# Kernel tuning notes

Measured on AMD Instinct MI355X. Metric: run time of the kernel, lower is better.

## Reference

```python
import jax, jax.numpy as jnp
import numpy as np

N_SAMPLES = 131072
N_EVENTS = 128
N_ATOMS = 32
ATOM_SIZE = 512
LATENT_DIM = 16
TOTAL_LAYERS = 7  # log2(n_events)


def setup_inputs() -> dict:
    key = jax.random.key(0)
    ks = jax.random.split(key, 9)
    r = lambda k, s: jax.random.normal(k, s, dtype=jnp.float32) * 0.1
    return {
        "base_latent": r(ks[0], (1, LATENT_DIM)),
        "to_off_w": r(ks[1], (TOTAL_LAYERS, 2, LATENT_DIM)),
        "split_w": r(ks[2], (TOTAL_LAYERS, 2 * LATENT_DIM, LATENT_DIM)),
        "split_b": r(ks[3], (TOTAL_LAYERS, 2 * LATENT_DIM)),
        "atoms": r(ks[4], (N_ATOMS, ATOM_SIZE)),
        "to_atoms_w": r(ks[5], (N_ATOMS, LATENT_DIM)),
        "to_atoms_b": r(ks[6], (N_ATOMS,)),
        "to_amp_w": r(ks[7], (1, LATENT_DIM)),
        "to_amp_b": r(ks[8], (1,)),
    }


def fft_shift(a, shift):
    # FFT-based fractional delay: pad to 3*n, phase-rotate spectrum, crop.
    n = a.shape[-1]
    shift_samples = shift * n * 0.5  # shift: (B, E, 1)
    a = jnp.pad(a, [(0, 0)] * (a.ndim - 1) + [(0, n * 2)])
    spec = jnp.fft.rfft(a, axis=-1, norm="ortho")
    n_coeffs = spec.shape[-1]
    coeffs = (jnp.arange(n_coeffs) * 2j * jnp.pi) / n_coeffs  # (n_coeffs,)
    spec = spec * jnp.exp(coeffs * shift_samples)  # broadcast (B,E,n_coeffs)
    samples = jnp.fft.irfft(spec, axis=-1, norm="ortho")
    return samples[..., :n]


def _forward(base_latent, to_off_w, split_w, split_b, atoms,
             to_atoms_w, to_atoms_b, to_amp_w, to_amp_b):
    x = base_latent[:, None, :]                     # (1, 1, L)
    base_times = jnp.zeros((1, 1, 1), dtype=x.dtype)
    for i in range(TOTAL_LAYERS):
        scale = 1.0 / (2 ** i)
        b, e, _ = x.shape
        to = jax.nn.sigmoid(jnp.einsum("bel,ol->beo", x, to_off_w[i]))  # (b,e,2)
        base_times = (base_times + to * scale).reshape(b, e * 2, 1)
        split = jnp.einsum("bel,ol->beo", x, split_w[i]) + split_b[i]   # (b,e,2L)
        x = split.reshape(b, e * 2, LATENT_DIM)
    # x: (1, 128, L), base_times: (1, 128, 1)
    mix = jnp.einsum("bel,al->bea", x, to_atoms_w) + to_atoms_b          # (1,E,A)
    ev = jnp.einsum("bea,at->bet", mix, atoms)                           # (1,E,512)
    n_arr = jnp.arange(ATOM_SIZE, dtype=ev.dtype)
    window = 0.54 - 0.46 * jnp.cos(2.0 * jnp.pi * n_arr / ATOM_SIZE)     # periodic hamming
    ev = ev * window
    ev = jnp.pad(ev, ((0, 0), (0, 0), (0, N_SAMPLES - ATOM_SIZE)))       # (1,E,n_samples)
    ev = ev / (jnp.linalg.norm(ev, axis=-1, keepdims=True) + 1e-8)       # unit_norm
    amps = jnp.einsum("bel,ol->beo", x, to_amp_w) + to_amp_b             # (1,E,1)
    ev = ev * amps
    scheduled = fft_shift(ev, base_times)                                # (1,E,n_samples)
    return jnp.sum(scheduled, axis=1, keepdims=True)                     # (1,1,n_samples)


def reference(base_latent, to_off_w, split_w, split_b, atoms,
              to_atoms_w, to_atoms_b, to_amp_w, to_amp_b):
    return _forward(base_latent, to_off_w, split_w, split_b, atoms,
                    to_atoms_w, to_atoms_b, to_amp_w, to_amp_b)
```

## Files before the change

### kernel.cpp

```cpp
#include <hip/hip_runtime.h>
#include <hip/hip_bf16.h>
#include <math.h>

constexpr int NSAMP  = 131072;
constexpr int NEV    = 128;
constexpr int ASIZE  = 512;
constexpr int LDIM   = 16;
constexpr int NLAYER = 7;
constexpr int NFFT   = 393216;
constexpr int MHALF  = 196608;
constexpr double TWO_PI = 6.283185307179586;


__device__ __forceinline__ float2 cmulf(float2 a, float2 b) {
    return make_float2(a.x*b.x - a.y*b.y, a.x*b.y + a.y*b.x);
}
__device__ __forceinline__ float2 CADD(float2 a, float2 b){ return make_float2(a.x+b.x, a.y+b.y); }
__device__ __forceinline__ float2 CSUB(float2 a, float2 b){ return make_float2(a.x-b.x, a.y-b.y); }

__device__ __forceinline__ void phase_sc(float th32, float* ps, float* pc) {
    const double th = (double)th32;
    const double n  = rint(th * 0.15915494309189535);
    double r = fma(-n, 6.283185307179586, th);
    r = fma(-n, 2.4492935982947064e-16, r);
    __sincosf((float)r, ps, pc);
}

#define RT2 0.70710678118654752f
#define DFT8F(A0,A1,A2,A3,A4,A5,A6,A7, X0,X1,X2,X3,X4,X5,X6,X7) { \
  float2 b0=CADD(A0,A4), b1=CADD(A1,A5), b2=CADD(A2,A6), b3=CADD(A3,A7); \
  float2 c0=CSUB(A0,A4); \
  float2 d1=CSUB(A1,A5), d2=CSUB(A2,A6), d3=CSUB(A3,A7); \
  float2 c1=make_float2((d1.x+d1.y)*RT2, (d1.y-d1.x)*RT2); \
  float2 c2=make_float2(d2.y, -d2.x); \
  float2 c3=make_float2((d3.y-d3.x)*RT2, -(d3.x+d3.y)*RT2); \
  float2 t0=CADD(b0,b2), t1=CSUB(b0,b2), t2=CADD(b1,b3), t3=CSUB(b1,b3); \
  X0=CADD(t0,t2); X4=CSUB(t0,t2); \
  X2=make_float2(t1.x+t3.y, t1.y-t3.x); X6=make_float2(t1.x-t3.y, t1.y+t3.x); \
  t0=CADD(c0,c2); t1=CSUB(c0,c2); t2=CADD(c1,c3); t3=CSUB(c1,c3); \
  X1=CADD(t0,t2); X5=CSUB(t0,t2); \
  X3=make_float2(t1.x+t3.y, t1.y-t3.x); X7=make_float2(t1.x-t3.y, t1.y+t3.x); \
}

__global__ __launch_bounds__(256) void init_all(
    const float* __restrict__ base, const float* __restrict__ to_off_w,
    const float* __restrict__ split_w, const float* __restrict__ split_b,
    float* __restrict__ xF, float* __restrict__ sF,
    float2* __restrict__ Twf, float2* __restrict__ Ttab)
{
    const int blk = blockIdx.x;
    const int tid = threadIdx.x;
    if (blk == 0) {
        __shared__ float xA[NEV*LDIM], xB[NEV*LDIM], bA[NEV], bB[NEV];
        if (tid < LDIM) xA[tid] = base[tid];
        if (tid == 0) bA[0] = 0.0f;
        __syncthreads();
        float* xi = xA; float* xo = xB; float* bi = bA; float* bo = bB;
        for (int i = 0; i < NLAYER; ++i) {
            const int ein = 1 << i;
            const float scale = 1.0f / (float)(1 << i);
            for (int idx = tid; idx < ein*32; idx += 256) {
                const int ep = idx >> 5, o2 = idx & 31;
                const float* wr = split_w + (i*32 + o2)*LDIM;
                const float* xr = xi + ep*LDIM;
                float s = __fmul_rn(xr[0], wr[0]);
                for (int l = 1; l < LDIM; ++l)
                    s = __fadd_rn(s, __fmul_rn(xr[l], wr[l]));
                s = __fadd_rn(s, split_b[i*32 + o2]);
                xo[(ep*2 + (o2>>4))*LDIM + (o2&15)] = s;
            }
            for (int idx = tid; idx < ein*2; idx += 256) {
                const int ep = idx >> 1, o = idx & 1;
                const float* wr = to_off_w + (i*2 + o)*LDIM;
                const float* xr = xi + ep*LDIM;
                float v = __fmul_rn(xr[0], wr[0]);
                for (int l = 1; l < LDIM; ++l)
                    v = __fadd_rn(v, __fmul_rn(xr[l], wr[l]));
                const float ef = (float)exp(-(double)v);
                const float sg = __fdiv_rn(1.0f, __fadd_rn(1.0f, ef));
                bo[ep*2 + o] = __fadd_rn(bi[ep], __fmul_rn(sg, scale));
            }
            __syncthreads();
            float* t;
            t = xi; xi = xo; xo = t;
            t = bi; bi = bo; bo = t;
        }
        for (int idx = tid; idx < NEV*LDIM; idx += 256) xF[idx] = xi[idx];
        for (int e = tid; e < NEV; e += 256)
            sF[e] = __fmul_rn(__fmul_rn(bi[e], 131072.0f), 0.5f);
        return;
    }
    if (blk == 1) {
        double s, c;
        sincos(TWO_PI*(double)tid/256.0,   &s, &c); Twf[tid]       = make_float2((float)c,(float)s);
        sincos(TWO_PI*(double)tid/512.0,   &s, &c); Twf[256 + tid] = make_float2((float)c,(float)s);
        sincos(TWO_PI*(double)tid/768.0,   &s, &c); Twf[512 + tid] = make_float2((float)c,(float)s);
        sincos(TWO_PI*(double)tid/65536.0, &s, &c); Twf[768 + tid] = make_float2((float)c,(float)s);
        return;
    }
    const int b = blk - 2;
    for (int j = tid; j < 512; j += 256) {
        double s, c;
        sincos(-TWO_PI*(double)(b*j)/(double)NFFT, &s, &c);
        Ttab[b*512 + j] = make_float2((float)c, (float)s);
    }
}

__global__ __launch_bounds__(256) void events_f32(
    const float* __restrict__ atoms, const float* __restrict__ to_atoms_w,
    const float* __restrict__ to_atoms_b, const float* __restrict__ to_amp_w,
    const float* __restrict__ to_amp_b, const float* __restrict__ xF,
    float* __restrict__ zf)
{
    const int e = blockIdx.x;
    const int tid = threadIdx.x;
    __shared__ float mixS[32];
    __shared__ float evS[ASIZE];
    __shared__ double red[256];
    __shared__ float scl[2];
    const float* x = xF + e*LDIM;
    if (tid < 32) {
        const float* wr = to_atoms_w + tid*LDIM;
        float m = __fmul_rn(x[0], wr[0]);
        for (int l = 1; l < LDIM; ++l) m = __fadd_rn(m, __fmul_rn(x[l], wr[l]));
        mixS[tid] = __fadd_rn(m, to_atoms_b[tid]);
    }
    __syncthreads();
    double ss = 0.0;
    for (int u = tid; u < ASIZE; u += 256) {
        float v = __fmul_rn(mixS[0], atoms[u]);
        for (int a = 1; a < 32; ++a)
            v = __fadd_rn(v, __fmul_rn(mixS[a], atoms[a*ASIZE + u]));
        const float ang = __fdiv_rn(__fmul_rn(6.283185307179586f, (float)u), 512.0f);
        const float cw = (float)cos((double)ang);
        const float w  = __fsub_rn(0.54f, __fmul_rn(0.46f, cw));
        v = __fmul_rn(v, w);
        evS[u] = v;
        ss += (double)v * (double)v;
    }
    red[tid] = ss; __syncthreads();
    for (int s = 128; s > 0; s >>= 1) { if (tid < s) red[tid] += red[tid+s]; __syncthreads(); }
    if (tid == 0) {
        const float nf = (float)sqrt(red[0]);
        scl[0] = __fadd_rn(nf, 1e-8f);
        float a = __fmul_rn(x[0], to_amp_w[0]);
        for (int l = 1; l < LDIM; ++l) a = __fadd_rn(a, __fmul_rn(x[l], to_amp_w[l]));
        scl[1] = __fadd_rn(a, to_amp_b[0]);
    }
    __syncthreads();
    const float den = scl[0], amp = scl[1];
    for (int u = tid; u < ASIZE; u += 256)
        zf[e*ASIZE + u] = __fmul_rn(__fdiv_rn(evS[u], den), amp);
}

__global__ __launch_bounds__(256, 3) void forward_v2(
    const float* __restrict__ zf, const float* __restrict__ sF,
    const float2* __restrict__ Ttab, float* __restrict__ Hqf)
{
    __shared__ float2 FB[4*576];
    __shared__ float  sSh[32];
    const int b       = blockIdx.x >> 2;
    const int quarter = blockIdx.x & 3;
    const int tid  = threadIdx.x;
    const int wave = tid >> 6, lane = tid & 63;
    float2* F = FB + wave*576;
    const int e0 = quarter*32;
    const float2* Tg = Ttab + b*512;

    if (tid < 32) sSh[tid] = sF[e0 + tid];
    __syncthreads();

    float2 w0b, w1b;
    __sincosf(-6.283185307179586f/512.0f * (float)lane,        &w0b.y, &w0b.x);
    __sincosf(-6.283185307179586f/64.0f  * (float)(lane >> 3), &w1b.y, &w1b.x);

    float c2a[4], c2b[4];
    #pragma unroll
    for (int j = 0; j < 4; ++j) {
        const int a  = lane + 64*j;
        const int k1 = b + 768*a;
        const int k2 = (768 - b) + 768*(255 - a);
        c2a[j] = __fdiv_rn(__fmul_rn((float)(2*k1), 3.14159274101257324f), 196609.0f);
        c2b[j] = __fdiv_rn(__fmul_rn((float)(2*k2), 3.14159274101257324f), 196609.0f);
    }

    float a1R[4]={0,0,0,0}, a1I[4]={0,0,0,0};
    float a2R[4]={0,0,0,0}, a2I[4]={0,0,0,0};
    const int ph = lane + (lane >> 3);

    for (int it = 0; it < 8; ++it) {
        const int e = e0 + wave*8 + it;
        const float* zp = zf + e*ASIZE;
        {
            float2 i0,i1,i2,i3,i4,i5,i6,i7;
            {
                float z; float2 tt;
                z = zp[lane      ]; tt = Tg[lane      ]; i0 = make_float2(z*tt.x, z*tt.y);
                z = zp[lane +  64]; tt = Tg[lane +  64]; i1 = make_float2(z*tt.x, z*tt.y);
                z = zp[lane + 128]; tt = Tg[lane + 128]; i2 = make_float2(z*tt.x, z*tt.y);
                z = zp[lane + 192]; tt = Tg[lane + 192]; i3 = make_float2(z*tt.x, z*tt.y);
                z = zp[lane + 256]; tt = Tg[lane + 256]; i4 = make_float2(z*tt.x, z*tt.y);
                z = zp[lane + 320]; tt = Tg[lane + 320]; i5 = make_float2(z*tt.x, z*tt.y);
                z = zp[lane + 384]; tt = Tg[lane + 384]; i6 = make_float2(z*tt.x, z*tt.y);
                z = zp[lane + 448]; tt = Tg[lane + 448]; i7 = make_float2(z*tt.x, z*tt.y);
            }
            float2 x0,x1,x2,x3,x4,x5,x6,x7;
            DFT8F(i0,i1,i2,i3,i4,i5,i6,i7, x0,x1,x2,x3,x4,x5,x6,x7);
            const int ob = 9*lane;
            float2 wm = w0b;
            F[ob]   = x0;
            F[ob+1] = cmulf(x1, wm); wm = cmulf(wm, w0b);
            F[ob+2] = cmulf(x2, wm); wm = cmulf(wm, w0b);
            F[ob+3] = cmulf(x3, wm); wm = cmulf(wm, w0b);
            F[ob+4] = cmulf(x4, wm); wm = cmulf(wm, w0b);
            F[ob+5] = cmulf(x5, wm); wm = cmulf(wm, w0b);
            F[ob+6] = cmulf(x6, wm); wm = cmulf(wm, w0b);
            F[ob+7] = cmulf(x7, wm);
        }
        {
            const float2 i0 = F[ph      ], i1 = F[ph +  72], i2 = F[ph + 144],
                         i3 = F[ph + 216], i4 = F[ph + 288], i5 = F[ph + 360],
                         i6 = F[ph + 432], i7 = F[ph + 504];
            float2 x0,x1,x2,x3,x4,x5,x6,x7;
            DFT8F(i0,i1,i2,i3,i4,i5,i6,i7, x0,x1,x2,x3,x4,x5,x6,x7);
            const int q = lane & 7, p = lane >> 3;
            const int ob = q + 72*p;
            float2 wm = w1b;
            F[ob]    = x0;
            F[ob+ 9] = cmulf(x1, wm); wm = cmulf(wm, w1b);
            F[ob+18] = cmulf(x2, wm); wm = cmulf(wm, w1b);
            F[ob+27] = cmulf(x3, wm); wm = cmulf(wm, w1b);
            F[ob+36] = cmulf(x4, wm); wm = cmulf(wm, w1b);
            F[ob+45] = cmulf(x5, wm); wm = cmulf(wm, w1b);
            F[ob+54] = cmulf(x6, wm); wm = cmulf(wm, w1b);
            F[ob+63] = cmulf(x7, wm);
        }
        float2 Y[8];
        {
            const float2 i0 = F[ph      ], i1 = F[ph +  72], i2 = F[ph + 144],
                         i3 = F[ph + 216], i4 = F[ph + 288], i5 = F[ph + 360],
                         i6 = F[ph + 432], i7 = F[ph + 504];
            DFT8F(i0,i1,i2,i3,i4,i5,i6,i7, Y[0],Y[1],Y[2],Y[3],Y[4],Y[5],Y[6],Y[7]);
        }
        const float se = sSh[wave*8 + it];
        #pragma unroll
        for (int j = 0; j < 4; ++j) {
            float ps, pc;
            const float2 S0 = Y[j];
            phase_sc(__fmul_rn(c2a[j], se), &ps, &pc);
            a1R[j] = fmaf(S0.x, pc, fmaf(-S0.y, ps, a1R[j]));
            a1I[j] = fmaf(S0.x, ps, fmaf( S0.y, pc, a1I[j]));
            const float2 S1 = Y[j+4];
            phase_sc(__fmul_rn(c2b[j], se), &ps, &pc);
            a2R[j] = fmaf(S1.x, pc, fmaf( S1.y, ps, a2R[j]));
            a2I[j] = fmaf(S1.x, ps, fmaf(-S1.y, pc, a2I[j]));
        }
    }

    float* redF = (float*)FB;
    #pragma unroll
    for (int round = 0; round < 2; ++round) {
        __syncthreads();
        const int j0 = 2*round;
        float* my = redF + (wave*64 + lane)*8;
        my[0]=a1R[j0];   my[1]=a1I[j0];   my[2]=a2R[j0];   my[3]=a2I[j0];
        my[4]=a1R[j0+1]; my[5]=a1I[j0+1]; my[6]=a2R[j0+1]; my[7]=a2I[j0+1];
        __syncthreads();
        const int s = tid >> 2, c = tid & 3;
        #pragma unroll
        for (int jr = 0; jr < 2; ++jr) {
            float v = 0.f;
            #pragma unroll
            for (int w = 0; w < 4; ++w) v += redF[(w*64 + s)*8 + jr*4 + c];
            const int as = s + 64*(j0 + jr);
            if (c < 2) {
                Hqf[2*(quarter*196609 + b*256 + as) + c] = v;
            } else if (b != 384) {
                if (b != 0)
                    Hqf[2*(quarter*196609 + (768-b)*256 + (255-as)) + (c-2)] = v;
                else if (as == 0)
                    Hqf[2*(quarter*196609 + 196608) + (c-2)] = v;
            }
        }
    }
}

__device__ __forceinline__ void ifft256f_stage(
    const float2* __restrict__ src, float2* __restrict__ dst, int t, int s4,
    const float2* __restrict__ Tw256f)
{
    const int lg = 2*s4, st = 1 << lg;
    const int q = t & (st-1), p = t >> lg;
    const float2 A0 = src[t], A1 = src[t+64], A2 = src[t+128], A3 = src[t+192];
    const float Pr = A0.x + A2.x, Pi_ = A0.y + A2.y;
    const float Qr = A0.x - A2.x, Qi  = A0.y - A2.y;
    const float Rr = A1.x + A3.x, Ri  = A1.y + A3.y;
    const float Sr = A1.x - A3.x, Si  = A1.y - A3.y;
    const int tw = p*st;
    const float2 w1 = Tw256f[tw];
    const float2 w2 = Tw256f[(2*tw) & 255];
    const float2 w3 = Tw256f[(3*tw) & 255];
    const int o = q + 4*st*p;
    dst[o] = make_float2(Pr + Rr, Pi_ + Ri);
    const float u1r = Qr - Si, u1i = Qi + Sr;
    dst[o + st]   = make_float2(u1r*w1.x - u1i*w1.y, u1r*w1.y + u1i*w1.x);
    const float u2r = Pr - Rr, u2i = Pi_ - Ri;
    dst[o + 2*st] = make_float2(u2r*w2.x - u2i*w2.y, u2r*w2.y + u2i*w2.x);
    const float u3r = Qr + Si, u3i = Qi - Sr;
    dst[o + 3*st] = make_float2(u3r*w3.x - u3i*w3.y, u3r*w3.y + u3i*w3.x);
}

__global__ __launch_bounds__(64) void inv_a(
    const float* __restrict__ Hqf, const float2* __restrict__ Twf,
    float2* __restrict__ Yg)
{
    __shared__ float2 buf[512];
    const int t = threadIdx.x;
    const int job = blockIdx.x;
    const int l = job >> 8, j1 = job & 255;
    const int k0 = 3*j1 + l;
    float2* A = buf; float2* B = buf + 256;
    const float2* Hq2 = (const float2*)Hqf;
    const float2* Tw256f = Twf;
    const float2* Tw512f = Twf + 256;
    const float2* Tw64kf = Twf + 768;

    double Ss, Sc; sincos(TWO_PI*(double)k0/(double)NFFT, &Ss, &Sc);
    const float Scf = (float)Sc, Ssf = (float)Ss;

    #pragma unroll
    for (int r = 0; r < 4; ++r) {
        const int j2 = t + 64*r;
        const int idxK = k0*256 + j2;
        int idxM;
        if (k0 > 0) idxM = (768 - k0)*256 + (255 - j2);
        else        idxM = (j2 == 0) ? 196608 : (256 - j2);
        float hkR=0.f, hkI=0.f, hmR=0.f, hmI=0.f;
        #pragma unroll
        for (int q = 0; q < 4; ++q) {
            const float2 vk = Hq2[q*196609 + idxK];
            const float2 vm = Hq2[q*196609 + idxM];
            hkR += vk.x; hkI += vk.y;
            hmR += vm.x; hmI += vm.y;
        }
        if (k0 == 0 && j2 == 0) { hkI = 0.f; hmI = 0.f; }
        const float Pr = hkR + hmR, Pi_ = hkI - hmI;
        const float Qr = hkR - hmR, Qi = hkI + hmI;
        const float2 t5 = Tw512f[j2];
        const float Wc = Scf*t5.x - Ssf*t5.y;
        const float Wsn = Scf*t5.y + Ssf*t5.x;
        const float WQr = Wc*Qr - Wsn*Qi;
        const float WQi = Wc*Qi + Wsn*Qr;
        A[j2] = make_float2(0.5f*(Pr - WQi), 0.5f*(Pi_ + WQr));
    }

    ifft256f_stage(A, B, t, 0, Tw256f);
    ifft256f_stage(B, A, t, 1, Tw256f);
    ifft256f_stage(A, B, t, 2, Tw256f);
    ifft256f_stage(B, A, t, 3, Tw256f);

    #pragma unroll
    for (int r = 0; r < 4; ++r) {
        const int m1 = t + 64*r;
        const float2 v = A[m1];
        const int vv = j1*m1;
        const float2 wa = Tw256f[vv >> 8];
        const float2 wb = Tw64kf[vv & 255];
        const float twc = wa.x*wb.x - wa.y*wb.y;
        const float tws = wa.x*wb.y + wa.y*wb.x;
        Yg[m1*768 + job] = make_float2(v.x*twc - v.y*tws, v.x*tws + v.y*twc);
    }
}

__global__ __launch_bounds__(192) void inv_b(
    const float2* __restrict__ Yg, const float2* __restrict__ Twf,
    float* __restrict__ out)
{
    __shared__ float2 buf[3*512];
    const int m1 = blockIdx.x;
    const int tid = threadIdx.x;
    const int l = tid >> 6, t = tid & 63;
    const float2* Tw256f = Twf;
    const float2* Tw768f = Twf + 512;
    {
        float2* A = buf + l*512;
        float2* B = A + 256;
        #pragma unroll
        for (int r = 0; r < 4; ++r) {
            const int j1 = t + 64*r;
            A[j1] = Yg[m1*768 + l*256 + j1];
        }
        ifft256f_stage(A, B, t, 0, Tw256f);
        ifft256f_stage(B, A, t, 1, Tw256f);
        ifft256f_stage(A, B, t, 2, Tw256f);
        ifft256f_stage(B, A, t, 3, Tw256f);
    }
    __syncthreads();

    double smd, cmd; sincos(TWO_PI*(double)m1/(double)MHALF, &smd, &cmd);
    const float cm = (float)cmd, sm = (float)smd;
    const float inv = 1.0f/(float)MHALF;
    for (int m2 = tid; m2 < 256; m2 += 192) {
        const float2 F0 = buf[m2];
        const float2 F1 = buf[512 + m2];
        const float2 F2 = buf[1024 + m2];
        const float2 t7 = Tw768f[m2];
        const float w1c = cm*t7.x - sm*t7.y, w1s = cm*t7.y + sm*t7.x;
        const float w2c = w1c*w1c - w1s*w1s, w2s = 2.0f*w1c*w1s;
        const float gr = F0.x + (w1c*F1.x - w1s*F1.y) + (w2c*F2.x - w2s*F2.y);
        const float gi = F0.y + (w1c*F1.y + w1s*F1.x) + (w2c*F2.y + w2s*F2.x);
        const int m = m1 + 256*m2;
        out[2*m]     = gr*inv;
        out[2*m + 1] = gi*inv;
    }
}

extern "C" void kernel_launch(void* const* d_in, const int* in_sizes, int n_in,
                              void* d_out, int out_size, void* d_ws, size_t ws_size,
                              hipStream_t stream) {
    const float* base       = (const float*)d_in[0];
    const float* to_off_w   = (const float*)d_in[1];
    const float* split_w    = (const float*)d_in[2];
    const float* split_b    = (const float*)d_in[3];
    const float* atoms      = (const float*)d_in[4];
    const float* to_atoms_w = (const float*)d_in[5];
    const float* to_atoms_b = (const float*)d_in[6];
    const float* to_amp_w   = (const float*)d_in[7];
    const float* to_amp_b   = (const float*)d_in[8];
    float* out = (float*)d_out;

    char* ws = (char*)d_ws;
    float2* Twf  = (float2*)(ws + 0);
    float*  sF   = (float*)(ws + 8192);
    float*  xF   = (float*)(ws + 8704);
    float*  zf   = (float*)(ws + 16896);
    float2* Ttab = (float2*)(ws + 279040);
    float2* Yg   = (float2*)(ws + 279040);
    float*  Hqf  = (float*)(ws + 1856000);

    init_all<<<387, 256, 0, stream>>>(base, to_off_w, split_w, split_b,
                                      xF, sF, Twf, Ttab);
    events_f32<<<NEV, 256, 0, stream>>>(atoms, to_atoms_w, to_atoms_b,
                                        to_amp_w, to_amp_b, xF, zf);
    forward_v2<<<385*4, 256, 0, stream>>>(zf, sF, Ttab, Hqf);
    inv_a<<<768, 64, 0, stream>>>(Hqf, Twf, Yg);
    inv_b<<<256, 192, 0, stream>>>(Yg, Twf, out);
}
```

Measured before the change: 138.8 us.

## Transpose z and twiddle layouts for vector loads, hoist twiddles, prefetch next event

The event buffer and the per-bin twiddle table are now stored interleaved so that each lane's eight strided inputs sit contiguously. The forward kernel can then fetch them with float4 loads instead of sixteen scalar and float2 loads. The twiddle values are loaded once into registers outside the event loop, and the next event's samples are prefetched during the current DFT. The shared shift array and its barrier are replaced by direct global reads, and launch bounds are raised to four blocks per SU. The intent is to cut global load instructions and hide load latency, at the cost of extra register pressure that could cause spills under the tighter occupancy bound.

```diff
diff --git a/kernel.cpp b/kernel.cpp
--- a/kernel.cpp
+++ b/kernel.cpp
@@ -102,7 +102,7 @@
     for (int j = tid; j < 512; j += 256) {
         double s, c;
         sincos(-TWO_PI*(double)(b*j)/(double)NFFT, &s, &c);
-        Ttab[b*512 + j] = make_float2((float)c, (float)s);
+        Ttab[b*512 + (j & 63)*8 + (j >> 6)] = make_float2((float)c, (float)s);
     }
 }
 
@@ -150,25 +150,28 @@
     __syncthreads();
     const float den = scl[0], amp = scl[1];
     for (int u = tid; u < ASIZE; u += 256)
-        zf[e*ASIZE + u] = __fmul_rn(__fdiv_rn(evS[u], den), amp);
-}
-
-__global__ __launch_bounds__(256, 3) void forward_v2(
+        zf[e*ASIZE + (u & 63)*8 + (u >> 6)] =
+            __fmul_rn(__fdiv_rn(evS[u], den), amp);
+}
+
+__global__ __launch_bounds__(256, 4) void forward_v3(
     const float* __restrict__ zf, const float* __restrict__ sF,
     const float2* __restrict__ Ttab, float* __restrict__ Hqf)
 {
     __shared__ float2 FB[4*576];
-    __shared__ float  sSh[32];
     const int b       = blockIdx.x >> 2;
     const int quarter = blockIdx.x & 3;
     const int tid  = threadIdx.x;
     const int wave = tid >> 6, lane = tid & 63;
     float2* F = FB + wave*576;
     const int e0 = quarter*32;
-    const float2* Tg = Ttab + b*512;
-
-    if (tid < 32) sSh[tid] = sF[e0 + tid];
-    __syncthreads();
+
+    const float4* Tg4 = (const float4*)(Ttab + b*512 + lane*8);
+    const float4 tA = Tg4[0], tB = Tg4[1], tC = Tg4[2], tD = Tg4[3];
+    const float2 T0 = make_float2(tA.x, tA.y), T1 = make_float2(tA.z, tA.w);
+    const float2 T2 = make_float2(tB.x, tB.y), T3 = make_float2(tB.z, tB.w);
+    const float2 T4 = make_float2(tC.x, tC.y), T5 = make_float2(tC.z, tC.w);
+    const float2 T6 = make_float2(tD.x, tD.y), T7 = make_float2(tD.z, tD.w);
 
     float2 w0b, w1b;
     __sincosf(-6.283185307179586f/512.0f * (float)lane,        &w0b.y, &w0b.x);
@@ -188,22 +191,22 @@
     float a2R[4]={0,0,0,0}, a2I[4]={0,0,0,0};
     const int ph = lane + (lane >> 3);
 
+    const float4* zp4 = (const float4*)(zf + (e0 + wave*8)*ASIZE + lane*8);
+    float4 za = zp4[0], zb = zp4[1];
+
     for (int it = 0; it < 8; ++it) {
-        const int e = e0 + wave*8 + it;
-        const float* zp = zf + e*ASIZE;
+        const float sev = sF[e0 + wave*8 + it];
         {
-            float2 i0,i1,i2,i3,i4,i5,i6,i7;
-            {
-                float z; float2 tt;
-                z = zp[lane      ]; tt = Tg[lane      ]; i0 = make_float2(z*tt.x, z*tt.y);
-                z = zp[lane +  64]; tt = Tg[lane +  64]; i1 = make_float2(z*tt.x, z*tt.y);
-                z = zp[lane + 128]; tt = Tg[lane + 128]; i2 = make_float2(z*tt.x, z*tt.y);
-                z = zp[lane + 192]; tt = Tg[lane + 192]; i3 = make_float2(z*tt.x, z*tt.y);
-                z = zp[lane + 256]; tt = Tg[lane + 256]; i4 = make_float2(z*tt.x, z*tt.y);
-                z = zp[lane + 320]; tt = Tg[lane + 320]; i5 = make_float2(z*tt.x, z*tt.y);
-                z = zp[lane + 384]; tt = Tg[lane + 384]; i6 = make_float2(z*tt.x, z*tt.y);
-                z = zp[lane + 448]; tt = Tg[lane + 448]; i7 = make_float2(z*tt.x, z*tt.y);
-            }
+            const float2 i0 = make_float2(za.x*T0.x, za.x*T0.y);
+            const float2 i1 = make_float2(za.y*T1.x, za.y*T1.y);
+            const float2 i2 = make_float2(za.z*T2.x, za.z*T2.y);
+            const float2 i3 = make_float2(za.w*T3.x, za.w*T3.y);
+            const float2 i4 = make_float2(zb.x*T4.x, zb.x*T4.y);
+            const float2 i5 = make_float2(zb.y*T5.x, zb.y*T5.y);
+            const float2 i6 = make_float2(zb.z*T6.x, zb.z*T6.y);
+            const float2 i7 = make_float2(zb.w*T7.x, zb.w*T7.y);
+            za = zp4[(it+1)*128];
+            zb = zp4[(it+1)*128 + 1];
             float2 x0,x1,x2,x3,x4,x5,x6,x7;
             DFT8F(i0,i1,i2,i3,i4,i5,i6,i7, x0,x1,x2,x3,x4,x5,x6,x7);
             const int ob = 9*lane;
@@ -242,16 +245,15 @@
                          i6 = F[ph + 432], i7 = F[ph + 504];
             DFT8F(i0,i1,i2,i3,i4,i5,i6,i7, Y[0],Y[1],Y[2],Y[3],Y[4],Y[5],Y[6],Y[7]);
         }
-        const float se = sSh[wave*8 + it];
         #pragma unroll
         for (int j = 0; j < 4; ++j) {
             float ps, pc;
             const float2 S0 = Y[j];
-            phase_sc(__fmul_rn(c2a[j], se), &ps, &pc);
+            phase_sc(__fmul_rn(c2a[j], sev), &ps, &pc);
             a1R[j] = fmaf(S0.x, pc, fmaf(-S0.y, ps, a1R[j]));
             a1I[j] = fmaf(S0.x, ps, fmaf( S0.y, pc, a1I[j]));
             const float2 S1 = Y[j+4];
-            phase_sc(__fmul_rn(c2b[j], se), &ps, &pc);
+            phase_sc(__fmul_rn(c2b[j], sev), &ps, &pc);
             a2R[j] = fmaf(S1.x, pc, fmaf( S1.y, ps, a2R[j]));
             a2I[j] = fmaf(S1.x, ps, fmaf(-S1.y, pc, a2I[j]));
         }
@@ -442,7 +444,7 @@
                                       xF, sF, Twf, Ttab);
     events_f32<<<NEV, 256, 0, stream>>>(atoms, to_atoms_w, to_atoms_b,
                                         to_amp_w, to_amp_b, xF, zf);
-    forward_v2<<<385*4, 256, 0, stream>>>(zf, sF, Ttab, Hqf);
+    forward_v3<<<385*4, 256, 0, stream>>>(zf, sF, Ttab, Hqf);
     inv_a<<<768, 64, 0, stream>>>(Hqf, Twf, Yg);
     inv_b<<<256, 192, 0, stream>>>(Yg, Twf, out);
 }
```

Result: slower. 145.2 us (+4.6%).
